# Kernel optimization log

Measured on AMD Instinct MI355X. Metric: run time of the kernel, lower is better.

Reference implementation:

```python
import jax, jax.numpy as jnp
import numpy as np

N = 100_000   # n_unique_nodes
E = 200_000   # temporal edges
MEM = 172     # memory_dim == node feature dim
FEAT = 172
TD = 100      # time encoding dim
K = 10        # n_degree sampled neighbors
H = 2         # attention heads
DH = MEM // H
MSG = 2 * MEM + FEAT + TD  # identity message dim = 616


def setup_inputs() -> dict:
    key = jax.random.key(0)
    ks = jax.random.split(key, 24)
    s = 0.05
    return {
        "node_features": jax.random.normal(ks[0], (N, FEAT), jnp.float32),
        "memory": jax.random.normal(ks[1], (N, MEM), jnp.float32) * 0.1,
        "last_update": jnp.zeros((N,), jnp.float32),
        "timestamps": jnp.sort(jax.random.uniform(ks[2], (E,), jnp.float32) * 1e4),
        "edge_features": jax.random.normal(ks[3], (E, FEAT), jnp.float32),
        "neighbor_ts": jax.random.uniform(ks[4], (N, K), jnp.float32) * 1e4,
        "time_w": jax.random.normal(ks[5], (TD,), jnp.float32),
        "time_b": jax.random.normal(ks[6], (TD,), jnp.float32),
        "gru_Wi": jax.random.normal(ks[7], (3 * MEM, MSG), jnp.float32) * s,
        "gru_Wh": jax.random.normal(ks[8], (3 * MEM, MEM), jnp.float32) * s,
        "gru_bi": jnp.zeros((3 * MEM,), jnp.float32),
        "gru_bh": jnp.zeros((3 * MEM,), jnp.float32),
        "Wq": jax.random.normal(ks[9], (MEM + TD, MEM), jnp.float32) * s,
        "Wk": jax.random.normal(ks[10], (MEM + TD, MEM), jnp.float32) * s,
        "Wv": jax.random.normal(ks[11], (MEM + TD, MEM), jnp.float32) * s,
        "W1": jax.random.normal(ks[12], (2 * MEM, MEM), jnp.float32) * s,
        "b1": jnp.zeros((MEM,), jnp.float32),
        "W2": jax.random.normal(ks[13], (MEM, MEM), jnp.float32) * s,
        "b2": jnp.zeros((MEM,), jnp.float32),
        "fc2_w": jax.random.normal(ks[14], (MEM, 2), jnp.float32) * s,
        "fc2_b": jnp.zeros((2,), jnp.float32),
        "sources": jax.random.randint(ks[15], (E,), 0, N),
        "destinations": jax.random.randint(ks[16], (E,), 0, N),
        "neighbor_idx": jax.random.randint(ks[17], (N, K), 0, N),
    }


def reference(node_features, memory, last_update, timestamps, edge_features,
              neighbor_ts, time_w, time_b, gru_Wi, gru_Wh, gru_bi, gru_bh,
              Wq, Wk, Wv, W1, b1, W2, b2, fc2_w, fc2_b,
              sources, destinations, neighbor_idx):
    tenc = lambda t: jnp.cos(t[..., None] * time_w + time_b)  # [..., TD]

    # ---- identity messages for both endpoints of each temporal edge ----
    mem_s, mem_d = memory[sources], memory[destinations]
    dts = timestamps - last_update[sources]
    dtd = timestamps - last_update[destinations]
    msg_s = jnp.concatenate([mem_s, mem_d, edge_features, tenc(dts)], axis=1)
    msg_d = jnp.concatenate([mem_d, mem_s, edge_features, tenc(dtd)], axis=1)
    msgs = jnp.concatenate([msg_s, msg_d], axis=0)          # [2E, MSG]
    node_ids = jnp.concatenate([sources, destinations])      # [2E]
    ts2 = jnp.concatenate([timestamps, timestamps])

    # ---- 'last' aggregator: keep most recent message per node ----
    pos = jnp.arange(2 * E, dtype=jnp.int32)
    last_pos = jax.ops.segment_max(pos, node_ids, num_segments=N)
    has_msg = last_pos >= 0                                  # empty segs -> int min
    safe = jnp.maximum(last_pos, 0)
    m = msgs[safe]                                           # [N, MSG]
    t_node = ts2[safe]

    # ---- GRU memory updater ----
    gi = m @ gru_Wi.T + gru_bi
    gh = memory @ gru_Wh.T + gru_bh
    r = jax.nn.sigmoid(gi[:, :MEM] + gh[:, :MEM])
    z = jax.nn.sigmoid(gi[:, MEM:2 * MEM] + gh[:, MEM:2 * MEM])
    n = jnp.tanh(gi[:, 2 * MEM:] + r * gh[:, 2 * MEM:])
    h_new = (1.0 - z) * n + z * memory
    memory_upd = jnp.where(has_msg[:, None], h_new, memory)  # [N, MEM]

    # ---- temporal graph attention embedding (1 layer, H heads, K neighbors) ----
    h = memory_upd + node_features                           # [N, MEM]
    t_now = timestamps[-1]
    q_in = jnp.concatenate([h, tenc(jnp.zeros((N,), h.dtype))], axis=1)   # [N, MEM+TD]
    n_h = h[neighbor_idx]                                    # [N, K, MEM]
    k_in = jnp.concatenate([n_h, tenc(t_now - neighbor_ts)], axis=2)     # [N, K, MEM+TD]
    q = (q_in @ Wq).reshape(N, H, DH)
    k = (k_in @ Wk).reshape(N, K, H, DH)
    v = (k_in @ Wv).reshape(N, K, H, DH)
    scores = jnp.einsum('nhd,nkhd->nhk', q, k) / np.sqrt(DH).astype(np.float32)
    attn = jax.nn.softmax(scores, axis=-1)
    agg = jnp.einsum('nhk,nkhd->nhd', attn, v).reshape(N, MEM)
    emb = jnp.maximum(jnp.concatenate([h, agg], axis=1) @ W1 + b1, 0.0) @ W2 + b2

    # ---- classifier head (visible part of Net.forward) ----
    out_feature = jnp.mean(emb[1:], axis=0)                  # skip padding node 0
    logits = jnp.tanh(out_feature) @ fc2_w + fc2_b
    return jax.nn.softmax(logits.reshape(1, -1), axis=1)
```

## Files before the change

kernel.cpp:

```cpp
#include <hip/hip_runtime.h>
#include <hip/hip_bf16.h>
#include <math.h>

#define NND 100000
#define NED 200000
#define MROWS 100096

using bf16 = __hip_bfloat16;
using short8 = __attribute__((ext_vector_type(8))) short;
using f32x4  = __attribute__((ext_vector_type(4))) float;

typedef __attribute__((address_space(3))) void lds_t;
typedef __attribute__((address_space(1))) const void gv_t;
__device__ __forceinline__ void gl16(const void* g, void* l) {
  __builtin_amdgcn_global_load_lds((gv_t*)g, (lds_t*)l, 16, 0, 0);
}

__device__ __forceinline__ float bfs2f(short s) {
  union { unsigned u; float f; } v; v.u = ((unsigned)(unsigned short)s) << 16; return v.f;
}
__device__ __forceinline__ short f2bfs(float f) {
  bf16 b = __float2bfloat16(f);
  union { bf16 b; short s; } u; u.b = b; return u.s;
}

#define INV2PI 0.15915494309189533577f

__device__ __forceinline__ float cos_rev(float r) {
  r = r - floorf(r);
  return __builtin_amdgcn_cosf(r);
}
__device__ __forceinline__ float fast_exp(float x) { return __expf(x); }
__device__ __forceinline__ float fast_rcp(float x) { return __builtin_amdgcn_rcpf(x); }
__device__ __forceinline__ float fast_sigmoid(float x) {
  return __builtin_amdgcn_rcpf(1.f + __expf(-x));
}
__device__ __forceinline__ float fast_tanh(float x) {
  float e = __expf(2.f * fabsf(x));
  float t = 1.f - 2.f * __builtin_amdgcn_rcpf(e + 1.f);
  return copysignf(t, x);
}


__global__ void init_k(int* lastpos, float* relu_sum) {
  int i = blockIdx.x * 256 + threadIdx.x;
  if (i < NND) lastpos[i] = -1;
  if (i < 172) relu_sum[i] = 0.f;
}

__global__ void scatter_k(const int* __restrict__ src, const int* __restrict__ dst,
                          int* lastpos) {
  int e = blockIdx.x * 256 + threadIdx.x;
  if (e < NED) {
    atomicMax(&lastpos[src[e]], e);
    atomicMax(&lastpos[dst[e]], NED + e);
  }
}

__global__ void meta_k(const int* __restrict__ lastpos,
                       const int* __restrict__ src, const int* __restrict__ dst,
                       const float* __restrict__ ts, const float* __restrict__ last_update,
                       int* other, int* edge, float* dtv, int* hasm) {
  int n = blockIdx.x * 256 + threadIdx.x;
  if (n >= NND) return;
  int p = lastpos[n];
  int oth = n, e = 0, hm = 0;
  float d = 0.f;
  if (p >= 0) {
    hm = 1;
    if (p >= NED) { e = p - NED; oth = src[e]; }
    else          { e = p;       oth = dst[e]; }
    d = ts[e] - last_update[n];
  }
  other[n] = oth; edge[n] = e; dtv[n] = d; hasm[n] = hm;
}

__global__ void qbias_k(const float* __restrict__ tb, const float* __restrict__ Wq,
                        float* qbias) {
  int o = threadIdx.x;
  if (o < 172) {
    float s = 0.f;
    for (int d = 0; d < 100; d++) s += cosf(tb[d]) * Wq[(172 + d) * 172 + o];
    qbias[o] = s;
  }
}

__global__ void bias716_k(const float* __restrict__ qbias, const float* __restrict__ Wk,
                          float* bias) {
  int o = blockIdx.x * 256 + threadIdx.x;
  if (o >= 716) return;
  float v = 0.f;
  if (o < 172) v = qbias[o];
  else if (o >= 516) {
    int p = o - 516, hh = p / 100, d = p - hh * 100;
    const float* qb  = qbias + hh * 86;
    const float* wk2 = Wk + (172 + d) * 172 + hh * 86;
    float s = 0.f;
    for (int cc = 0; cc < 86; cc++) s = fmaf(qb[cc], wk2[cc], s);
    v = s;
  }
  bias[o] = v;
}

__global__ void cvtW_k(const float* __restrict__ src, bf16* __restrict__ dst,
                       int R, int S, int r, int s) {
  int i = blockIdx.x * 256 + threadIdx.x;
  if (i >= R * S) return;
  int rr = i / S, cc = i - rr * S;
  float v = (rr < r && cc < s) ? src[(size_t)rr * s + cc] : 0.f;
  dst[i] = __float2bfloat16(v);
}

__global__ void packBT_k(const float* __restrict__ Wq, const float* __restrict__ Wk,
                         const float* __restrict__ Wv, bf16* __restrict__ dst) {
  int i = blockIdx.x * 256 + threadIdx.x;
  if (i >= 768 * 192) return;
  int o = i / 192, c = i - o * 192;
  float v = 0.f;
  if (o < 716 && c < 172) {
    if (o < 172)      v = Wq[c * 172 + o];
    else if (o < 344) v = Wk[c * 172 + (o - 172)];
    else if (o < 516) v = Wv[c * 172 + (o - 344)];
    else {
      int p = o - 516, hh = p / 100, d = p - hh * 100;
      const float* wq  = Wq + c * 172 + hh * 86;
      const float* wk2 = Wk + (172 + d) * 172 + hh * 86;
      float s = 0.f;
      for (int cc = 0; cc < 86; cc++) s = fmaf(wq[cc], wk2[cc], s);
      v = s;
    }
  }
  dst[i] = __float2bfloat16(v);
}

__global__ void packW1x_k(const float* __restrict__ W1, const float* __restrict__ Wv,
                          bf16* __restrict__ dst) {
  int i = blockIdx.x * 256 + threadIdx.x;
  if (i >= 256 * 544) return;
  int o = i / 544, k = i - o * 544;
  float v = 0.f;
  if (o < 172) {
    if (k < 344) v = W1[(size_t)k * 172 + o];
    else {
      int p = k - 344, hh = p / 100, d = p - hh * 100;
      const float* wv2 = Wv + (size_t)(172 + d) * 172;
      float s = 0.f;
      for (int t = hh * 86; t < hh * 86 + 86; t++)
        s = fmaf(wv2[t], W1[(size_t)(172 + t) * 172 + o], s);
      v = s;
    }
  }
  dst[i] = __float2bfloat16(v);
}

__global__ void msg_k(const float* __restrict__ mem, const float* __restrict__ ef,
                      const int* __restrict__ other, const int* __restrict__ edge,
                      const float* __restrict__ dtv, const float* __restrict__ tw,
                      const float* __restrict__ tb, bf16* __restrict__ Mg) {
  int i = blockIdx.x * 256 + threadIdx.x;
  if (i >= MROWS * 640) return;
  int n = i / 640, c = i - n * 640;
  float v = 0.f;
  if (n < NND && c < 616) {
    if (c < 172)      v = mem[(size_t)n * 172 + c];
    else if (c < 344) v = mem[(size_t)other[n] * 172 + (c - 172)];
    else if (c < 516) v = ef[(size_t)edge[n] * 172 + (c - 344)];
    else              v = cos_rev(fmaf(dtv[n], tw[c - 516] * INV2PI, tb[c - 516] * INV2PI));
  }
  Mg[i] = __float2bfloat16(v);
}

__global__ void cvtmem_k(const float* __restrict__ mem, bf16* __restrict__ dst) {
  int i = blockIdx.x * 256 + threadIdx.x;
  if (i >= MROWS * 192) return;
  int n = i / 192, c = i - n * 192;
  float v = (n < NND && c < 172) ? mem[(size_t)n * 172 + c] : 0.f;
  dst[i] = __float2bfloat16(v);
}

__global__ void padrow_k(bf16* __restrict__ haw) {
  int i = blockIdx.x * 256 + threadIdx.x;
  if (i < (MROWS - NND) * 544) haw[(size_t)NND * 544 + i] = __float2bfloat16(0.f);
}

__global__ void gru_k(const bf16* __restrict__ gi, const bf16* __restrict__ gh,
                      const float* __restrict__ memory, const float* __restrict__ nf,
                      const int* __restrict__ hasm,
                      bf16* __restrict__ hB, bf16* __restrict__ haw) {
  int i = blockIdx.x * 256 + threadIdx.x;
  if (i >= MROWS * 192) return;
  int n = i / 192, c = i - n * 192;
  if (n >= NND || c >= 172) { hB[i] = __float2bfloat16(0.f); return; }
  float memv = memory[(size_t)n * 172 + c];
  float hv = memv;
  if (hasm[n]) {
    const bf16* gin = gi + (size_t)n * 516;
    const bf16* ghn = gh + (size_t)n * 516;
    float r  = fast_sigmoid(__bfloat162float(gin[c]) + __bfloat162float(ghn[c]));
    float z  = fast_sigmoid(__bfloat162float(gin[172 + c]) + __bfloat162float(ghn[172 + c]));
    float nn = fast_tanh(__bfloat162float(gin[344 + c]) + r * __bfloat162float(ghn[344 + c]));
    hv = (1.f - z) * nn + z * memv;
  }
  float hout = hv + nf[(size_t)n * 172 + c];
  bf16 hb = __float2bfloat16(hout);
  hB[i] = hb;
  haw[(size_t)n * 544 + c] = hb;
}


template<int EPI>
__global__ __launch_bounds__(256) void mgemm_k(
    const bf16* __restrict__ A, int AS, const bf16* __restrict__ B, int BS,
    const float* __restrict__ bias,
    float* __restrict__ C, int CS, bf16* __restrict__ Cb, int CbS,
    float* __restrict__ red, int M, int O, int K) {
  __shared__ bf16 As[128 * 32];
  __shared__ bf16 Bs[128 * 32];
  const int tid = threadIdx.x, w = tid >> 6, lane = tid & 63;
  const int m0 = blockIdx.x * 128, o0 = blockIdx.y * 128;
  const int quad = lane >> 4, l16 = lane & 15;
  const int wm = (w & 1) * 64, wn = (w >> 1) * 64;
  f32x4 acc[4][4] = {};
  const bf16* ga = A + (size_t)(m0 + w * 32 + (lane >> 2)) * AS + (lane & 3) * 8;
  const bf16* gb = B + (size_t)(o0 + w * 32 + (lane >> 2)) * BS + (lane & 3) * 8;
  bf16* lA = As + w * 1024;
  bf16* lB = Bs + w * 1024;
  for (int k0 = 0; k0 < K; k0 += 32) {
    gl16(ga, lA);               gl16(ga + (size_t)16 * AS, lA + 512);
    gl16(gb, lB);               gl16(gb + (size_t)16 * BS, lB + 512);
    ga += 32; gb += 32;
    __syncthreads();
    short8 af[4], bfm[4];
    #pragma unroll
    for (int i = 0; i < 4; i++)
      af[i] = *(const short8*)&As[(wm + i * 16 + l16) * 32 + quad * 8];
    #pragma unroll
    for (int j = 0; j < 4; j++)
      bfm[j] = *(const short8*)&Bs[(wn + j * 16 + l16) * 32 + quad * 8];
    #pragma unroll
    for (int i = 0; i < 4; i++)
      #pragma unroll
      for (int j = 0; j < 4; j++)
        acc[i][j] = __builtin_amdgcn_mfma_f32_16x16x32_bf16(af[i], bfm[j], acc[i][j], 0, 0, 0);
    __syncthreads();
  }
  if (EPI == 2) {
    #pragma unroll
    for (int i = 0; i < 4; i++)
      #pragma unroll
      for (int p = 0; p < 4; p++) {
        const int m = m0 + wm + i * 16 + quad * 4 + p;
        if (m < M) {
          #pragma unroll
          for (int j = 0; j < 4; j++) {
            const int o = o0 + wn + j * 16 + l16;
            if (o < O) Cb[(size_t)m * CbS + o] = __float2bfloat16(acc[i][j][p] + bias[o]);
          }
        }
      }
  } else if (EPI == 3) {
    #pragma unroll
    for (int i = 0; i < 4; i++)
      #pragma unroll
      for (int p = 0; p < 4; p++) {
        const int m = m0 + wm + i * 16 + quad * 4 + p;
        if (m < M) {
          #pragma unroll
          for (int j = 0; j < 4; j++) {
            const int o = o0 + wn + j * 16 + l16;
            if (o < O) {
              const float v = acc[i][j][p] + bias[o];
              if (o < 172)      C[(size_t)m * CS + o] = v;
              else if (o < 516) Cb[(size_t)m * CbS + (o - 172)] = __float2bfloat16(v);
              else              C[(size_t)m * CS + (o - 344)] = v;
            }
          }
        }
      }
  } else {
    __shared__ float colsum[128];
    if (tid < 128) colsum[tid] = 0.f;
    __syncthreads();
    float part[4] = {0.f, 0.f, 0.f, 0.f};
    #pragma unroll
    for (int i = 0; i < 4; i++)
      #pragma unroll
      for (int p = 0; p < 4; p++) {
        const int m = m0 + wm + i * 16 + quad * 4 + p;
        const bool valid = (m < M) && (m != 0);
        if (valid) {
          #pragma unroll
          for (int j = 0; j < 4; j++) {
            const int o = o0 + wn + j * 16 + l16;
            if (o < O) part[j] += fmaxf(acc[i][j][p] + bias[o], 0.f);
          }
        }
      }
    #pragma unroll
    for (int j = 0; j < 4; j++) atomicAdd(&colsum[wn + j * 16 + l16], part[j]);
    __syncthreads();
    if (tid < 128) {
      const int o = o0 + tid;
      if (o < O) atomicAdd(&red[o], colsum[tid]);
    }
  }
}

__global__ __launch_bounds__(256) void attn3_k(
    const float* __restrict__ Cq, const bf16* __restrict__ kv,
    const float* __restrict__ tw, const float* __restrict__ tb,
    const int* __restrict__ nidx, const float* __restrict__ nts,
    const float* __restrict__ ts, bf16* __restrict__ haw) {
  const int w = threadIdx.x >> 6, lane = threadIdx.x & 63;
  const int wid = blockIdx.x * 4 + w;
  const float t_now = ts[NED - 1];
  const float* row = Cq + (size_t)wid * 372;

  float qs0[8], qs1[8];
  {
    float qc[8];
    if (lane < 22) {
      float4 a = *(const float4*)(row + 8 * lane);
      float4 b = *(const float4*)(row + 8 * lane + 4);
      qc[0] = a.x; qc[1] = a.y; qc[2] = a.z; qc[3] = a.w;
      qc[4] = b.x; qc[5] = b.y; qc[6] = b.z; qc[7] = b.w;
    } else {
      #pragma unroll
      for (int p = 0; p < 8; p++) qc[p] = 0.f;
    }
    #pragma unroll
    for (int p = 0; p < 8; p++) {
      const int e = 8 * lane + p;
      qs0[p] = (e < 86) ? qc[p] : 0.f;
      qs1[p] = (e >= 86 && e < 172) ? qc[p] : 0.f;
    }
  }
  const float k0a = row[172 + lane];
  const float k0b = (lane < 36) ? row[236 + lane] : 0.f;
  const float k1a = row[272 + lane];
  const float k1b = (lane < 36) ? row[336 + lane] : 0.f;
  const float twa = tw[lane] * INV2PI, tba = tb[lane] * INV2PI;
  const float twb = (lane < 36) ? tw[64 + lane] * INV2PI : 0.f;
  const float tbb = (lane < 36) ? tb[64 + lane] * INV2PI : 0.f;

  short8 kvc[10];
  float ta[10], tbv[10], s0[10], s1[10];
  #pragma unroll
  for (int j = 0; j < 10; j++) {
    const int ix = nidx[wid * 10 + j];
    const float ndt = t_now - nts[wid * 10 + j];
    const float tja = cos_rev(fmaf(ndt, twa, tba));
    const float tjb = (lane < 36) ? cos_rev(fmaf(ndt, twb, tbb)) : 0.f;
    ta[j] = tja; tbv[j] = tjb;
    short8 c = {0, 0, 0, 0, 0, 0, 0, 0};
    if (lane < 43) c = *(const short8*)(kv + (size_t)ix * 344 + 8 * lane);
    kvc[j] = c;
    float p0 = tja * k0a + tjb * k0b;
    float p1 = tja * k1a + tjb * k1b;
    #pragma unroll
    for (int p = 0; p < 8; p++) {
      const float hvv = bfs2f(c[p]);
      p0 = fmaf(qs0[p], hvv, p0);
      p1 = fmaf(qs1[p], hvv, p1);
    }
    #pragma unroll
    for (int off = 32; off; off >>= 1) {
      p0 += __shfl_xor(p0, off);
      p1 += __shfl_xor(p1, off);
    }
    const float scale = 0.10783277320343841f;
    s0[j] = p0 * scale; s1[j] = p1 * scale;
  }
  float m0 = s0[0], m1v = s1[0];
  #pragma unroll
  for (int j = 1; j < 10; j++) { m0 = fmaxf(m0, s0[j]); m1v = fmaxf(m1v, s1[j]); }
  float z0 = 0.f, z1 = 0.f;
  #pragma unroll
  for (int j = 0; j < 10; j++) {
    s0[j] = fast_exp(s0[j] - m0);  z0 += s0[j];
    s1[j] = fast_exp(s1[j] - m1v); z1 += s1[j];
  }
  const float i0 = fast_rcp(z0), i1 = fast_rcp(z1);
  float av0[8] = {}, av1[8] = {};
  float w0a = 0.f, w0b = 0.f, w1a = 0.f, w1b = 0.f;
  #pragma unroll
  for (int j = 0; j < 10; j++) {
    const float a0 = s0[j] * i0, a1 = s1[j] * i1;
    #pragma unroll
    for (int p = 0; p < 8; p++) {
      const float hvv = bfs2f(kvc[j][p]);
      av0[p] = fmaf(a0, hvv, av0[p]);
      av1[p] = fmaf(a1, hvv, av1[p]);
    }
    w0a = fmaf(a0, ta[j], w0a); w0b = fmaf(a0, tbv[j], w0b);
    w1a = fmaf(a1, ta[j], w1a); w1b = fmaf(a1, tbv[j], w1b);
  }
  bf16* hrow = haw + (size_t)wid * 544;
  if (lane >= 22 && lane < 43) {
    short8 st;
    #pragma unroll
    for (int p = 0; p < 8; p++) {
      const int e = 8 * lane + p;
      st[p] = f2bfs((e < 258) ? av0[p] : av1[p]);
    }
    *(short8*)(hrow + 8 * lane) = st;
  } else if (lane == 21) {
    #pragma unroll
    for (int p = 4; p < 8; p++) hrow[168 + p] = __float2bfloat16(av0[p]);
  }
  hrow[344 + lane] = __float2bfloat16(w0a);
  if (lane < 36) hrow[408 + lane] = __float2bfloat16(w0b);
  hrow[444 + lane] = __float2bfloat16(w1a);
  if (lane < 36) hrow[508 + lane] = __float2bfloat16(w1b);
}


__global__ void head_k(const float* __restrict__ relu_sum, const float* __restrict__ W2,
                       const float* __restrict__ b2, const float* __restrict__ fc2w,
                       const float* __restrict__ fc2b, float* out) {
  __shared__ float th[172];
  int t = threadIdx.x;
  if (t < 172) {
    float s = 0.f;
    for (int c = 0; c < 172; c++) s = fmaf(relu_sum[c], W2[c * 172 + t], s);
    s = s * (1.0f / 99999.0f) + b2[t];
    th[t] = tanhf(s);
  }
  __syncthreads();
  if (t == 0) {
    float l0 = fc2b[0], l1 = fc2b[1];
    for (int o = 0; o < 172; o++) {
      l0 = fmaf(th[o], fc2w[o * 2 + 0], l0);
      l1 = fmaf(th[o], fc2w[o * 2 + 1], l1);
    }
    float mx = fmaxf(l0, l1);
    float e0 = expf(l0 - mx), e1 = expf(l1 - mx);
    float inv = 1.f / (e0 + e1);
    out[0] = e0 * inv;
    out[1] = e1 * inv;
  }
}


extern "C" void kernel_launch(void* const* d_in, const int* in_sizes, int n_in,
                              void* d_out, int out_size, void* d_ws, size_t ws_size,
                              hipStream_t stream) {
  (void)in_sizes; (void)n_in; (void)out_size;
  const float* node_features = (const float*)d_in[0];
  const float* memory        = (const float*)d_in[1];
  const float* last_update   = (const float*)d_in[2];
  const float* timestamps    = (const float*)d_in[3];
  const float* edge_features = (const float*)d_in[4];
  const float* neighbor_ts   = (const float*)d_in[5];
  const float* time_w        = (const float*)d_in[6];
  const float* time_b        = (const float*)d_in[7];
  const float* gru_Wi        = (const float*)d_in[8];
  const float* gru_Wh        = (const float*)d_in[9];
  const float* gru_bi        = (const float*)d_in[10];
  const float* gru_bh        = (const float*)d_in[11];
  const float* Wq            = (const float*)d_in[12];
  const float* Wk            = (const float*)d_in[13];
  const float* Wv            = (const float*)d_in[14];
  const float* W1            = (const float*)d_in[15];
  const float* b1            = (const float*)d_in[16];
  const float* W2            = (const float*)d_in[17];
  const float* b2            = (const float*)d_in[18];
  const float* fc2_w         = (const float*)d_in[19];
  const float* fc2_b         = (const float*)d_in[20];
  const int* sources         = (const int*)d_in[21];
  const int* destinations    = (const int*)d_in[22];
  const int* neighbor_idx    = (const int*)d_in[23];
  float* out = (float*)d_out;

  float* F = (float*)d_ws;
  int*   I = (int*)d_ws;
  size_t off = 0;
  auto alloc = [&off](size_t words) { size_t r = off; off += (words + 63) & ~(size_t)63; return r; };
  const size_t w_lastpos = alloc(NND);
  const size_t w_other   = alloc(NND);
  const size_t w_edge    = alloc(NND);
  const size_t w_dtv     = alloc(NND);
  const size_t w_hasm    = alloc(NND);
  const size_t w_qbias   = alloc(172);
  const size_t w_b716    = alloc(716);
  const size_t w_relu    = alloc(172);
  const size_t w_WiB     = alloc(640 * 640 / 2);
  const size_t w_WhB     = alloc(640 * 192 / 2);
  const size_t w_pBT     = alloc(768 * 192 / 2);
  const size_t w_W1x     = alloc(256 * 544 / 2);
  const size_t w_R1 = alloc((size_t)NND * 372);
  const size_t w_R2 = alloc((size_t)NND * 516 / 2);
  const size_t w_R4 = alloc((size_t)MROWS * 192 / 2);
  const size_t w_R5 = alloc((size_t)MROWS * 544 / 2);
  if (ws_size < off * 4) return;

  int*   lastpos = I + w_lastpos;
  int*   other   = I + w_other;
  int*   edge    = I + w_edge;
  float* dtv     = F + w_dtv;
  int*   hasm    = I + w_hasm;
  float* qbias   = F + w_qbias;
  float* b716    = F + w_b716;
  float* relu_s  = F + w_relu;
  bf16*  WiB     = (bf16*)(F + w_WiB);
  bf16*  WhB     = (bf16*)(F + w_WhB);
  bf16*  pBT     = (bf16*)(F + w_pBT);
  bf16*  W1x     = (bf16*)(F + w_W1x);
  bf16*  Mg      = (bf16*)(F + w_R1);
  bf16*  ghB     = (bf16*)(F + w_R1);
  float* Cq      = F + w_R1;
  bf16*  giB     = (bf16*)(F + w_R2);
  bf16*  kvB     = (bf16*)(F + w_R2);
  bf16*  memB    = (bf16*)(F + w_R4);
  bf16*  hB      = (bf16*)(F + w_R4);
  bf16*  haw     = (bf16*)(F + w_R5);

  init_k<<<(NND + 255) / 256, 256, 0, stream>>>(lastpos, relu_s);
  scatter_k<<<(NED + 255) / 256, 256, 0, stream>>>(sources, destinations, lastpos);
  meta_k<<<(NND + 255) / 256, 256, 0, stream>>>(lastpos, sources, destinations,
                                                timestamps, last_update,
                                                other, edge, dtv, hasm);
  qbias_k<<<1, 256, 0, stream>>>(time_b, Wq, qbias);
  bias716_k<<<3, 256, 0, stream>>>(qbias, Wk, b716);
  cvtW_k<<<(640 * 640 + 255) / 256, 256, 0, stream>>>(gru_Wi, WiB, 640, 640, 516, 616);
  cvtW_k<<<(640 * 192 + 255) / 256, 256, 0, stream>>>(gru_Wh, WhB, 640, 192, 516, 172);
  packBT_k<<<(768 * 192 + 255) / 256, 256, 0, stream>>>(Wq, Wk, Wv, pBT);
  packW1x_k<<<(256 * 544 + 255) / 256, 256, 0, stream>>>(W1, Wv, W1x);
  msg_k<<<(MROWS * 640) / 256, 256, 0, stream>>>(memory, edge_features, other, edge,
                                                 dtv, time_w, time_b, Mg);
  cvtmem_k<<<(MROWS * 192) / 256, 256, 0, stream>>>(memory, memB);
  padrow_k<<<((MROWS - NND) * 544 + 255) / 256, 256, 0, stream>>>(haw);

  mgemm_k<2><<<dim3(782, 5), 256, 0, stream>>>(Mg, 640, WiB, 640, gru_bi,
                                               nullptr, 0, giB, 516, nullptr,
                                               NND, 516, 640);
  mgemm_k<2><<<dim3(782, 5), 256, 0, stream>>>(memB, 192, WhB, 192, gru_bh,
                                               nullptr, 0, ghB, 516, nullptr,
                                               NND, 516, 192);
  gru_k<<<(MROWS * 192) / 256, 256, 0, stream>>>(giB, ghB, memory, node_features,
                                                 hasm, hB, haw);
  mgemm_k<3><<<dim3(782, 6), 256, 0, stream>>>(hB, 192, pBT, 192, b716,
                                               Cq, 372, kvB, 344, nullptr,
                                               NND, 716, 192);
  attn3_k<<<NND / 4, 256, 0, stream>>>(Cq, kvB, time_w, time_b,
                                       neighbor_idx, neighbor_ts, timestamps, haw);
  mgemm_k<1><<<dim3(782, 2), 256, 0, stream>>>(haw, 544, W1x, 544, b1,
                                               nullptr, 0, nullptr, 0, relu_s,
                                               NND, 172, 544);
  head_k<<<1, 256, 0, stream>>>(relu_s, W2, b2, fc2_w, fc2_b, out);
}
```

Measured before the change: 1.750 ms.

## Vectorize message/GRU kernels, swap GEMM grid order, pad KV rows, prefetch attention gathers

```diff
diff --git a/kernel.cpp b/kernel.cpp
--- a/kernel.cpp
+++ b/kernel.cpp
@@ -8,6 +8,7 @@
 
 using bf16 = __hip_bfloat16;
 using short8 = __attribute__((ext_vector_type(8))) short;
+using short4v = __attribute__((ext_vector_type(4))) short;
 using f32x4  = __attribute__((ext_vector_type(4))) float;
 
 typedef __attribute__((address_space(3))) void lds_t;
@@ -42,10 +43,15 @@
 }
 
 
-__global__ void init_k(int* lastpos, float* relu_sum) {
+__global__ void init_k(int* lastpos, float* relu_sum, const float* __restrict__ tw,
+                       const float* __restrict__ tb, float* twp, float* tbp) {
   int i = blockIdx.x * 256 + threadIdx.x;
   if (i < NND) lastpos[i] = -1;
   if (i < 172) relu_sum[i] = 0.f;
+  if (i < 128) {
+    twp[i] = (i < 100) ? tw[i] * INV2PI : 0.f;
+    tbp[i] = (i < 100) ? tb[i] * INV2PI : 0.f;
+  }
 }
 
 __global__ void scatter_k(const int* __restrict__ src, const int* __restrict__ dst,
@@ -153,21 +159,53 @@
   dst[i] = __float2bfloat16(v);
 }
 
-__global__ void msg_k(const float* __restrict__ mem, const float* __restrict__ ef,
-                      const int* __restrict__ other, const int* __restrict__ edge,
-                      const float* __restrict__ dtv, const float* __restrict__ tw,
-                      const float* __restrict__ tb, bf16* __restrict__ Mg) {
-  int i = blockIdx.x * 256 + threadIdx.x;
-  if (i >= MROWS * 640) return;
-  int n = i / 640, c = i - n * 640;
-  float v = 0.f;
+__global__ void msg2_k(const float* __restrict__ mem, const float* __restrict__ ef,
+                       const int* __restrict__ other, const int* __restrict__ edge,
+                       const float* __restrict__ dtv, const float* __restrict__ twp,
+                       const float* __restrict__ tbp, bf16* __restrict__ Mg) {
+  int i = blockIdx.x * 256 + threadIdx.x;
+  if (i >= MROWS * 80) return;
+  int n = i / 80, c8 = i - n * 80;
+  int c = c8 * 8;
+  short8 st = {0, 0, 0, 0, 0, 0, 0, 0};
   if (n < NND && c < 616) {
-    if (c < 172)      v = mem[(size_t)n * 172 + c];
-    else if (c < 344) v = mem[(size_t)other[n] * 172 + (c - 172)];
-    else if (c < 516) v = ef[(size_t)edge[n] * 172 + (c - 344)];
-    else              v = cos_rev(fmaf(dtv[n], tw[c - 516] * INV2PI, tb[c - 516] * INV2PI));
-  }
-  Mg[i] = __float2bfloat16(v);
+    float v[8];
+    if (c + 8 <= 172) {
+      float4 a = *(const float4*)(mem + (size_t)n * 172 + c);
+      float4 b = *(const float4*)(mem + (size_t)n * 172 + c + 4);
+      v[0]=a.x; v[1]=a.y; v[2]=a.z; v[3]=a.w; v[4]=b.x; v[5]=b.y; v[6]=b.z; v[7]=b.w;
+    } else if (c >= 176 && c + 8 <= 344) {
+      const float* src = mem + (size_t)other[n] * 172 + (c - 172);
+      float4 a = *(const float4*)(src);
+      float4 b = *(const float4*)(src + 4);
+      v[0]=a.x; v[1]=a.y; v[2]=a.z; v[3]=a.w; v[4]=b.x; v[5]=b.y; v[6]=b.z; v[7]=b.w;
+    } else if (c >= 344 && c + 8 <= 516) {
+      const float* src = ef + (size_t)edge[n] * 172 + (c - 344);
+      float4 a = *(const float4*)(src);
+      float4 b = *(const float4*)(src + 4);
+      v[0]=a.x; v[1]=a.y; v[2]=a.z; v[3]=a.w; v[4]=b.x; v[5]=b.y; v[6]=b.z; v[7]=b.w;
+    } else if (c >= 520) {
+      float d0 = dtv[n];
+      #pragma unroll
+      for (int p = 0; p < 8; p++)
+        v[p] = cos_rev(fmaf(d0, twp[c - 516 + p], tbp[c - 516 + p]));
+    } else {
+      float d0 = dtv[n];
+      #pragma unroll
+      for (int p = 0; p < 8; p++) {
+        int col = c + p;
+        float x;
+        if (col < 172)      x = mem[(size_t)n * 172 + col];
+        else if (col < 344) x = mem[(size_t)other[n] * 172 + (col - 172)];
+        else if (col < 516) x = ef[(size_t)edge[n] * 172 + (col - 344)];
+        else                x = cos_rev(fmaf(d0, twp[col - 516], tbp[col - 516]));
+        v[p] = x;
+      }
+    }
+    #pragma unroll
+    for (int p = 0; p < 8; p++) st[p] = f2bfs(v[p]);
+  }
+  *(short8*)(Mg + (size_t)n * 640 + c) = st;
 }
 
 __global__ void cvtmem_k(const float* __restrict__ mem, bf16* __restrict__ dst) {
@@ -183,28 +221,52 @@
   if (i < (MROWS - NND) * 544) haw[(size_t)NND * 544 + i] = __float2bfloat16(0.f);
 }
 
-__global__ void gru_k(const bf16* __restrict__ gi, const bf16* __restrict__ gh,
-                      const float* __restrict__ memory, const float* __restrict__ nf,
-                      const int* __restrict__ hasm,
-                      bf16* __restrict__ hB, bf16* __restrict__ haw) {
-  int i = blockIdx.x * 256 + threadIdx.x;
-  if (i >= MROWS * 192) return;
-  int n = i / 192, c = i - n * 192;
-  if (n >= NND || c >= 172) { hB[i] = __float2bfloat16(0.f); return; }
-  float memv = memory[(size_t)n * 172 + c];
-  float hv = memv;
+__global__ void padkv_k(bf16* __restrict__ kv) {
+  int i = blockIdx.x * 256 + threadIdx.x;
+  if (i >= NND * 21) return;
+  int n = i / 21, c8 = i - n * 21;
+  short8 z = {0, 0, 0, 0, 0, 0, 0, 0};
+  *(short8*)(kv + (size_t)n * 512 + 344 + 8 * c8) = z;
+}
+
+__global__ void gru2_k(const bf16* __restrict__ gi, const bf16* __restrict__ gh,
+                       const float* __restrict__ memory, const float* __restrict__ nf,
+                       const int* __restrict__ hasm,
+                       bf16* __restrict__ hB, bf16* __restrict__ haw) {
+  int i = blockIdx.x * 256 + threadIdx.x;
+  if (i >= MROWS * 48) return;
+  int n = i / 48, c = (i - n * 48) * 4;
+  short4v z4 = {0, 0, 0, 0};
+  if (n >= NND || c >= 172) {
+    *(short4v*)(hB + (size_t)n * 192 + c) = z4;
+    return;
+  }
+  float4 mv = *(const float4*)(memory + (size_t)n * 172 + c);
+  float hv[4] = {mv.x, mv.y, mv.z, mv.w};
   if (hasm[n]) {
-    const bf16* gin = gi + (size_t)n * 516;
-    const bf16* ghn = gh + (size_t)n * 516;
-    float r  = fast_sigmoid(__bfloat162float(gin[c]) + __bfloat162float(ghn[c]));
-    float z  = fast_sigmoid(__bfloat162float(gin[172 + c]) + __bfloat162float(ghn[172 + c]));
-    float nn = fast_tanh(__bfloat162float(gin[344 + c]) + r * __bfloat162float(ghn[344 + c]));
-    hv = (1.f - z) * nn + z * memv;
-  }
-  float hout = hv + nf[(size_t)n * 172 + c];
-  bf16 hb = __float2bfloat16(hout);
-  hB[i] = hb;
-  haw[(size_t)n * 544 + c] = hb;
+    const bf16* gin = gi + (size_t)n * 516 + c;
+    const bf16* ghn = gh + (size_t)n * 516 + c;
+    short4v g0 = *(const short4v*)(gin);
+    short4v g1 = *(const short4v*)(gin + 172);
+    short4v g2 = *(const short4v*)(gin + 344);
+    short4v h0 = *(const short4v*)(ghn);
+    short4v h1 = *(const short4v*)(ghn + 172);
+    short4v h2 = *(const short4v*)(ghn + 344);
+    #pragma unroll
+    for (int p = 0; p < 4; p++) {
+      float r  = fast_sigmoid(bfs2f(g0[p]) + bfs2f(h0[p]));
+      float zz = fast_sigmoid(bfs2f(g1[p]) + bfs2f(h1[p]));
+      float nn = fast_tanh(bfs2f(g2[p]) + r * bfs2f(h2[p]));
+      hv[p] = (1.f - zz) * nn + zz * hv[p];
+    }
+  }
+  float4 nfv = *(const float4*)(nf + (size_t)n * 172 + c);
+  float nfa[4] = {nfv.x, nfv.y, nfv.z, nfv.w};
+  short4v hb;
+  #pragma unroll
+  for (int p = 0; p < 4; p++) hb[p] = f2bfs(hv[p] + nfa[p]);
+  *(short4v*)(hB + (size_t)n * 192 + c) = hb;
+  *(short4v*)(haw + (size_t)n * 544 + c) = hb;
 }
 
 
@@ -217,7 +279,7 @@
   __shared__ bf16 As[128 * 32];
   __shared__ bf16 Bs[128 * 32];
   const int tid = threadIdx.x, w = tid >> 6, lane = tid & 63;
-  const int m0 = blockIdx.x * 128, o0 = blockIdx.y * 128;
+  const int m0 = blockIdx.y * 128, o0 = blockIdx.x * 128;
   const int quad = lane >> 4, l16 = lane & 15;
   const int wm = (w & 1) * 64, wn = (w >> 1) * 64;
   f32x4 acc[4][4] = {};
@@ -306,16 +368,27 @@
   }
 }
 
-__global__ __launch_bounds__(256) void attn3_k(
+__global__ __launch_bounds__(256) void attn4_k(
     const float* __restrict__ Cq, const bf16* __restrict__ kv,
-    const float* __restrict__ tw, const float* __restrict__ tb,
+    const float* __restrict__ twp, const float* __restrict__ tbp,
     const int* __restrict__ nidx, const float* __restrict__ nts,
     const float* __restrict__ ts, bf16* __restrict__ haw) {
   const int w = threadIdx.x >> 6, lane = threadIdx.x & 63;
-  const int wid = blockIdx.x * 4 + w;
+  const int wid = __builtin_amdgcn_readfirstlane(blockIdx.x * 4 + w);
   const float t_now = ts[NED - 1];
+
+  int ixs[10]; float ndt[10];
+  #pragma unroll
+  for (int j = 0; j < 10; j++) ixs[j] = nidx[wid * 10 + j];
+  #pragma unroll
+  for (int j = 0; j < 10; j++) ndt[j] = t_now - nts[wid * 10 + j];
+
+  short8 kvc[10];
+  #pragma unroll
+  for (int j = 0; j < 10; j++)
+    kvc[j] = *(const short8*)(kv + (size_t)ixs[j] * 512 + 8 * lane);
+
   const float* row = Cq + (size_t)wid * 372;
-
   float qs0[8], qs1[8];
   {
     float qc[8];
@@ -336,30 +409,30 @@
     }
   }
   const float k0a = row[172 + lane];
-  const float k0b = (lane < 36) ? row[236 + lane] : 0.f;
+  const float k0b_raw = row[236 + lane];
   const float k1a = row[272 + lane];
-  const float k1b = (lane < 36) ? row[336 + lane] : 0.f;
-  const float twa = tw[lane] * INV2PI, tba = tb[lane] * INV2PI;
-  const float twb = (lane < 36) ? tw[64 + lane] * INV2PI : 0.f;
-  const float tbb = (lane < 36) ? tb[64 + lane] * INV2PI : 0.f;
-
-  short8 kvc[10];
-  float ta[10], tbv[10], s0[10], s1[10];
+  const float k1b_raw = row[336 + lane];
+  const bool ln36 = (lane < 36);
+  const float k0b = ln36 ? k0b_raw : 0.f;
+  const float k1b = ln36 ? k1b_raw : 0.f;
+  const float twa = twp[lane],      tba = tbp[lane];
+  const float twb = twp[64 + lane], tbb = tbp[64 + lane];
+
+  float ta[10], tbv[10];
   #pragma unroll
   for (int j = 0; j < 10; j++) {
-    const int ix = nidx[wid * 10 + j];
-    const float ndt = t_now - nts[wid * 10 + j];
-    const float tja = cos_rev(fmaf(ndt, twa, tba));
-    const float tjb = (lane < 36) ? cos_rev(fmaf(ndt, twb, tbb)) : 0.f;
-    ta[j] = tja; tbv[j] = tjb;
-    short8 c = {0, 0, 0, 0, 0, 0, 0, 0};
-    if (lane < 43) c = *(const short8*)(kv + (size_t)ix * 344 + 8 * lane);
-    kvc[j] = c;
-    float p0 = tja * k0a + tjb * k0b;
-    float p1 = tja * k1a + tjb * k1b;
+    ta[j]  = cos_rev(fmaf(ndt[j], twa, tba));
+    tbv[j] = cos_rev(fmaf(ndt[j], twb, tbb));
+  }
+
+  float s0[10], s1[10];
+  #pragma unroll
+  for (int j = 0; j < 10; j++) {
+    float p0 = ta[j] * k0a + tbv[j] * k0b;
+    float p1 = ta[j] * k1a + tbv[j] * k1b;
     #pragma unroll
     for (int p = 0; p < 8; p++) {
-      const float hvv = bfs2f(c[p]);
+      const float hvv = bfs2f(kvc[j][p]);
       p0 = fmaf(qs0[p], hvv, p0);
       p1 = fmaf(qs1[p], hvv, p1);
     }
@@ -409,9 +482,9 @@
     for (int p = 4; p < 8; p++) hrow[168 + p] = __float2bfloat16(av0[p]);
   }
   hrow[344 + lane] = __float2bfloat16(w0a);
-  if (lane < 36) hrow[408 + lane] = __float2bfloat16(w0b);
+  if (ln36) hrow[408 + lane] = __float2bfloat16(w0b);
   hrow[444 + lane] = __float2bfloat16(w1a);
-  if (lane < 36) hrow[508 + lane] = __float2bfloat16(w1b);
+  if (ln36) hrow[508 + lane] = __float2bfloat16(w1b);
 }
 
 
@@ -484,11 +557,13 @@
   const size_t w_qbias   = alloc(172);
   const size_t w_b716    = alloc(716);
   const size_t w_relu    = alloc(172);
+  const size_t w_twp     = alloc(128);
+  const size_t w_tbp     = alloc(128);
   const size_t w_WiB     = alloc(640 * 640 / 2);
   const size_t w_WhB     = alloc(640 * 192 / 2);
   const size_t w_pBT     = alloc(768 * 192 / 2);
   const size_t w_W1x     = alloc(256 * 544 / 2);
-  const size_t w_R1 = alloc((size_t)NND * 372);
+  const size_t w_R1 = alloc((size_t)NND * 372 + 256);
   const size_t w_R2 = alloc((size_t)NND * 516 / 2);
   const size_t w_R4 = alloc((size_t)MROWS * 192 / 2);
   const size_t w_R5 = alloc((size_t)MROWS * 544 / 2);
@@ -502,6 +577,8 @@
   float* qbias   = F + w_qbias;
   float* b716    = F + w_b716;
   float* relu_s  = F + w_relu;
+  float* twp     = F + w_twp;
+  float* tbp     = F + w_tbp;
   bf16*  WiB     = (bf16*)(F + w_WiB);
   bf16*  WhB     = (bf16*)(F + w_WhB);
   bf16*  pBT     = (bf16*)(F + w_pBT);
@@ -515,7 +592,7 @@
   bf16*  hB      = (bf16*)(F + w_R4);
   bf16*  haw     = (bf16*)(F + w_R5);
 
-  init_k<<<(NND + 255) / 256, 256, 0, stream>>>(lastpos, relu_s);
+  init_k<<<(NND + 255) / 256, 256, 0, stream>>>(lastpos, relu_s, time_w, time_b, twp, tbp);
   scatter_k<<<(NED + 255) / 256, 256, 0, stream>>>(sources, destinations, lastpos);
   meta_k<<<(NND + 255) / 256, 256, 0, stream>>>(lastpos, sources, destinations,
                                                 timestamps, last_update,
@@ -526,25 +603,26 @@
   cvtW_k<<<(640 * 192 + 255) / 256, 256, 0, stream>>>(gru_Wh, WhB, 640, 192, 516, 172);
   packBT_k<<<(768 * 192 + 255) / 256, 256, 0, stream>>>(Wq, Wk, Wv, pBT);
   packW1x_k<<<(256 * 544 + 255) / 256, 256, 0, stream>>>(W1, Wv, W1x);
-  msg_k<<<(MROWS * 640) / 256, 256, 0, stream>>>(memory, edge_features, other, edge,
-                                                 dtv, time_w, time_b, Mg);
+  msg2_k<<<(MROWS * 80) / 256, 256, 0, stream>>>(memory, edge_features, other, edge,
+                                                 dtv, twp, tbp, Mg);
   cvtmem_k<<<(MROWS * 192) / 256, 256, 0, stream>>>(memory, memB);
   padrow_k<<<((MROWS - NND) * 544 + 255) / 256, 256, 0, stream>>>(haw);
 
-  mgemm_k<2><<<dim3(782, 5), 256, 0, stream>>>(Mg, 640, WiB, 640, gru_bi,
+  mgemm_k<2><<<dim3(5, 782), 256, 0, stream>>>(Mg, 640, WiB, 640, gru_bi,
                                                nullptr, 0, giB, 516, nullptr,
                                                NND, 516, 640);
-  mgemm_k<2><<<dim3(782, 5), 256, 0, stream>>>(memB, 192, WhB, 192, gru_bh,
+  mgemm_k<2><<<dim3(5, 782), 256, 0, stream>>>(memB, 192, WhB, 192, gru_bh,
                                                nullptr, 0, ghB, 516, nullptr,
                                                NND, 516, 192);
-  gru_k<<<(MROWS * 192) / 256, 256, 0, stream>>>(giB, ghB, memory, node_features,
+  gru2_k<<<(MROWS * 48) / 256, 256, 0, stream>>>(giB, ghB, memory, node_features,
                                                  hasm, hB, haw);
-  mgemm_k<3><<<dim3(782, 6), 256, 0, stream>>>(hB, 192, pBT, 192, b716,
-                                               Cq, 372, kvB, 344, nullptr,
+  padkv_k<<<(NND * 21 + 255) / 256, 256, 0, stream>>>(kvB);
+  mgemm_k<3><<<dim3(6, 782), 256, 0, stream>>>(hB, 192, pBT, 192, b716,
+                                               Cq, 372, kvB, 512, nullptr,
                                                NND, 716, 192);
-  attn3_k<<<NND / 4, 256, 0, stream>>>(Cq, kvB, time_w, time_b,
+  attn4_k<<<NND / 4, 256, 0, stream>>>(Cq, kvB, twp, tbp,
                                        neighbor_idx, neighbor_ts, timestamps, haw);
-  mgemm_k<1><<<dim3(782, 2), 256, 0, stream>>>(haw, 544, W1x, 544, b1,
+  mgemm_k<1><<<dim3(2, 782), 256, 0, stream>>>(haw, 544, W1x, 544, b1,
                                                nullptr, 0, nullptr, 0, relu_s,
                                                NND, 172, 544);
   head_k<<<1, 256, 0, stream>>>(relu_s, W2, b2, fc2_w, fc2_b, out);
```

Result: faster. 1.442 ms (-17.6%).
